# Performance work log

Hardware: AMD Instinct MI355X
Metric: run time of the kernel (lower is better)

## Reference

```python
import jax, jax.numpy as jnp
import numpy as np
import math

B, T, C, H, D, R = 1, 2048, 2048, 16, 128, 64
W_LOCAL = 512
DELTA_I = 0.75
ROPE_BASE = 10000.0


def _rotate(x):
    # interleaved rotate-half, exactly as in the torch source
    x1, x2 = x[..., ::2], x[..., 1::2]
    return jnp.stack((-x2, x1), axis=-1).reshape(x.shape)


def _rope_tables(seq_len):
    inv_freq = 1.0 / (ROPE_BASE ** (jnp.arange(0, D, 2, dtype=jnp.float32) / D))
    t = jnp.arange(seq_len, dtype=jnp.float32)
    freqs = jnp.einsum('i,j->ij', t, inv_freq)          # [T, D/2]
    emb = jnp.concatenate((freqs, freqs), axis=-1)      # [T, D] (half-layout, as in source)
    return jnp.cos(emb)[None, None], jnp.sin(emb)[None, None]


def setup_inputs() -> dict:
    key = jax.random.key(0)
    ks = jax.random.split(key, 8)
    s = 0.02
    return {
        'x': jax.random.normal(ks[0], (B, T, C), dtype=jnp.float32),
        'w_qkv': jax.random.normal(ks[1], (3 * C, C), dtype=jnp.float32) * s,
        'w_o': jax.random.normal(ks[2], (C, C), dtype=jnp.float32) * s,
        'pk': jax.random.normal(ks[3], (R, D), dtype=jnp.float32) * s,
        'pv': jax.random.normal(ks[4], (R, D), dtype=jnp.float32) * s,
        'uo': jax.random.normal(ks[5], (D, R), dtype=jnp.float32) * s,
        'info_w1': jax.random.normal(ks[6], (C // 4, C), dtype=jnp.float32) * s,
        'info_w2': jax.random.normal(ks[7], (1, C // 4), dtype=jnp.float32) * s,
    }


def reference(x, w_qkv, w_o, pk, pv, uo, info_w1, info_w2):
    Bx, Tx, Cx = x.shape
    scale = 1.0 / math.sqrt(D)

    qkv = x @ w_qkv.T                                   # [B,T,3C]
    q, k, v = jnp.split(qkv, 3, axis=-1)
    q = q.reshape(Bx, Tx, H, D).transpose(0, 2, 1, 3)   # [B,H,T,D]
    k = k.reshape(Bx, Tx, H, D).transpose(0, 2, 1, 3)
    v = v.reshape(Bx, Tx, H, D).transpose(0, 2, 1, 3)

    cos, sin = _rope_tables(Tx)
    q = q * cos + _rotate(q) * sin
    k = k * cos + _rotate(k) * sin

    # causal local-window attention (full [B,H,T,T] scores, as in source)
    w = min(W_LOCAL, Tx)
    idx = jnp.arange(Tx)
    rel = idx[None, :] - idx[:, None]                   # j - i
    local_mask = (rel > 0) | (rel < -(w - 1))           # True = masked
    scores = jnp.einsum('bhtd,bhsd->bhts', q, k) * scale
    scores = jnp.where(local_mask[None, None], -jnp.inf, scores)
    attn_local = jax.nn.softmax(scores, axis=-1)
    ctx_local = jnp.einsum('bhts,bhsd->bhtd', attn_local, v)

    # informational gate (no-grad path in source)
    h_info = jax.nn.gelu(x @ info_w1.T, approximate=False)
    info_score = jax.nn.sigmoid((h_info @ info_w2.T)[..., 0])   # [B,T]
    gate = (info_score > DELTA_I).astype(x.dtype)

    # low-rank global path (unmasked softmax over all tokens, as in source)
    k_r = jnp.einsum('bhsd,rd->bhsr', k, pk)
    v_r = jnp.einsum('bhsd,rd->bhsr', v, pv)
    q_r = jnp.einsum('bhtd,rd->bhtr', q, pk)
    scores_g = jnp.einsum('bhtr,bhsr->bhts', q_r, k_r) * (scale * D / R)
    attn_g = jax.nn.softmax(scores_g, axis=-1)
    ctx_g_r = jnp.einsum('bhts,bhsr->bhtr', attn_g, v_r)
    ctx_g = jnp.einsum('bhtr,dr->bhtd', ctx_g_r, uo)
    gate_q = gate[:, None, :, None]                     # [B,1,T,1]
    ctx = ctx_local + ctx_g * gate_q

    ctx = ctx.transpose(0, 2, 1, 3).reshape(Bx, Tx, Cx)
    return ctx @ w_o.T
```

## Files before the change

### kernel.cpp

```cpp
#include <hip/hip_runtime.h>
#include <hip/hip_bf16.h>
#include <math.h>

#define T_LEN 2048
#define C_DIM 2048
#define NH 16
#define HD 128
#define RANK 64
#define W_LOCAL 512
#define QKV_LD 6144
#define ROW_BF 12288
#define KB_OFF 4096
#define VB_OFF 8192
#define WO_OFF 6144
#define SCALE 0.08838834764831845f
#define SCALE_G 0.17677669529663687f
#define LOG1E4_OVER_64 0.14391156831212787f

typedef __bf16 bf16_t;
typedef __bf16 bf16x8 __attribute__((ext_vector_type(8)));
typedef __bf16 bf16x4 __attribute__((ext_vector_type(4)));
typedef float f32x4 __attribute__((ext_vector_type(4)));

__device__ __forceinline__ void async_copy16(const bf16_t* g, bf16_t* l) {
    __builtin_amdgcn_global_load_lds(
        (const __attribute__((address_space(1))) unsigned int*)g,
        (__attribute__((address_space(3))) unsigned int*)l, 16, 0, 0);
}

__global__ __launch_bounds__(256)
void prep_kernel(const float* __restrict__ x, bf16_t* __restrict__ xb,
                 const float* __restrict__ w_qkv, bf16_t* __restrict__ wqb,
                 float* __restrict__ tab) {
    const int bid = blockIdx.x;
    const int tid = threadIdx.x;
    if (bid < 2048) {
        int idx = bid * 256 + tid;
        const float* p = x + (size_t)idx * 8;
        float4 v0 = *(const float4*)p;
        float4 v1 = *(const float4*)(p + 4);
        bf16x8 o;
        o[0] = (bf16_t)v0.x; o[1] = (bf16_t)v0.y; o[2] = (bf16_t)v0.z; o[3] = (bf16_t)v0.w;
        o[4] = (bf16_t)v1.x; o[5] = (bf16_t)v1.y; o[6] = (bf16_t)v1.z; o[7] = (bf16_t)v1.w;
        *(bf16x8*)(xb + (size_t)idx * 8) = o;
    } else if (bid < 8192) {
        int idx = (bid - 2048) * 256 + tid;
        const float* p = w_qkv + (size_t)idx * 8;
        float4 v0 = *(const float4*)p;
        float4 v1 = *(const float4*)(p + 4);
        bf16x8 o;
        o[0] = (bf16_t)v0.x; o[1] = (bf16_t)v0.y; o[2] = (bf16_t)v0.z; o[3] = (bf16_t)v0.w;
        o[4] = (bf16_t)v1.x; o[5] = (bf16_t)v1.y; o[6] = (bf16_t)v1.z; o[7] = (bf16_t)v1.w;
        *(bf16x8*)(wqb + (size_t)idx * 8) = o;
    } else {
        int idx = (bid - 8192) * 256 + tid;
        int t = idx >> 6, j = idx & 63;
        float inv = expf(-(float)j * LOG1E4_OVER_64);
        float s, c;
        sincosf((float)t * inv, &s, &c);
        tab[t * 128 + j] = c;
        tab[t * 128 + 64 + j] = s;
    }
}

#define NTK 32
#define ILD 40

#define STG_A(bb, ktile) do {                                                  \
    _Pragma("unroll")                                                          \
    for (int c_ = 0; c_ < 4; ++c_)                                             \
        async_copy16(gA + (size_t)(c_ * 32) * 2048 + (ktile) * 64,             \
                     &lds[bb][0][(c_ * 32 + rS) * 64 + dS]);                   \
} while (0)

#define STG_B(bb, ktile) do {                                                  \
    _Pragma("unroll")                                                          \
    for (int c_ = 0; c_ < 4; ++c_)                                             \
        async_copy16(gB + (size_t)(c_ * 32) * 2048 + (ktile) * 64,             \
                     &lds[bb][1][(c_ * 32 + rS) * 64 + dS]);                   \
} while (0)

#define RD_A(bb, m, k) (*(const bf16x8*)&lds[bb][0][(wr * 64 + (m) * 16 + l16) * 64 + (((k) * 4 + quad) ^ xsw) * 8])
#define RD_B(bb, n, k) (*(const bf16x8*)&lds[bb][1][(wc * 64 + (n) * 16 + l16) * 64 + (((k) * 4 + quad) ^ xsw) * 8])

__global__ __launch_bounds__(256, 2)
void gemm_qkv_rope(const bf16_t* __restrict__ A, const bf16_t* __restrict__ B,
                   bf16_t* __restrict__ qkv_bf, bf16_t* __restrict__ vt,
                   const float* __restrict__ tab, const float* __restrict__ w_o,
                   const float* __restrict__ x, const float* __restrict__ w1,
                   float* __restrict__ ipart) {
    __shared__ __align__(16) unsigned char smem[65536];
    const int bid = blockIdx.x;
    const int tid = threadIdx.x;

    if (bid < 128) {
        bf16_t* Ah = (bf16_t*)smem;
        bf16_t* Al = Ah + 128 * ILD;
        bf16_t* Bh = Al + 128 * ILD;
        bf16_t* Bl = Bh + 128 * ILD;
        const int bn = bid & 3, bm = (bid >> 2) & 15, ks = bid >> 6;
        const int wave = tid >> 6, lane = tid & 63;
        const int quad = lane >> 4, l16 = lane & 15;
        const int wm = (wave >> 1) * 64, wn = (wave & 1) * 64;
        const int lrow = lane >> 2;
        const int lkb = (lane & 3) * 8;
        const int kbeg = ks * 1024;

        f32x4 acc[4][4];
#pragma unroll
        for (int i = 0; i < 4; ++i)
#pragma unroll
            for (int j = 0; j < 4; ++j) acc[i][j] = (f32x4){0.f, 0.f, 0.f, 0.f};

        const float* gx = x + (size_t)(bm * 128 + wave * 16 + lrow) * 2048 + kbeg + lkb;
        const float* gw = w1 + (size_t)(bn * 128 + wave * 16 + lrow) * 2048 + kbeg + lkb;
        const int wrow = (wave * 16 + lrow) * ILD + lkb;

        for (int k0 = 0; k0 < 1024; k0 += 32) {
            __syncthreads();
#pragma unroll
            for (int hr = 0; hr < 2; ++hr) {
                const float* px = gx + (size_t)hr * 64 * 2048 + k0;
                float4 a0 = *(const float4*)px, a1 = *(const float4*)(px + 4);
                float av[8] = {a0.x, a0.y, a0.z, a0.w, a1.x, a1.y, a1.z, a1.w};
                bf16x8 h, l;
#pragma unroll
                for (int i = 0; i < 8; ++i) {
                    bf16_t hb = (bf16_t)av[i];
                    h[i] = hb; l[i] = (bf16_t)(av[i] - (float)hb);
                }
                *(bf16x8*)&Ah[wrow + hr * 64 * ILD] = h;
                *(bf16x8*)&Al[wrow + hr * 64 * ILD] = l;

                const float* pw = gw + (size_t)hr * 64 * 2048 + k0;
                float4 b0 = *(const float4*)pw, b1 = *(const float4*)(pw + 4);
                float bv[8] = {b0.x, b0.y, b0.z, b0.w, b1.x, b1.y, b1.z, b1.w};
                bf16x8 hb2, lb2;
#pragma unroll
                for (int i = 0; i < 8; ++i) {
                    bf16_t hh = (bf16_t)bv[i];
                    hb2[i] = hh; lb2[i] = (bf16_t)(bv[i] - (float)hh);
                }
                *(bf16x8*)&Bh[wrow + hr * 64 * ILD] = hb2;
                *(bf16x8*)&Bl[wrow + hr * 64 * ILD] = lb2;
            }
            __syncthreads();

            bf16x8 ah[4], al[4], bh[4], bl[4];
#pragma unroll
            for (int mt = 0; mt < 4; ++mt) {
                ah[mt] = *(const bf16x8*)&Ah[(wm + mt * 16 + l16) * ILD + quad * 8];
                al[mt] = *(const bf16x8*)&Al[(wm + mt * 16 + l16) * ILD + quad * 8];
            }
#pragma unroll
            for (int nt = 0; nt < 4; ++nt) {
                bh[nt] = *(const bf16x8*)&Bh[(wn + nt * 16 + l16) * ILD + quad * 8];
                bl[nt] = *(const bf16x8*)&Bl[(wn + nt * 16 + l16) * ILD + quad * 8];
            }
#pragma unroll
            for (int mt = 0; mt < 4; ++mt)
#pragma unroll
                for (int nt = 0; nt < 4; ++nt) {
                    acc[mt][nt] = __builtin_amdgcn_mfma_f32_16x16x32_bf16(ah[mt], bh[nt], acc[mt][nt], 0, 0, 0);
                    acc[mt][nt] = __builtin_amdgcn_mfma_f32_16x16x32_bf16(ah[mt], bl[nt], acc[mt][nt], 0, 0, 0);
                    acc[mt][nt] = __builtin_amdgcn_mfma_f32_16x16x32_bf16(al[mt], bh[nt], acc[mt][nt], 0, 0, 0);
                }
        }

        float* cp = ipart + (size_t)ks * 2048 * 512;
#pragma unroll
        for (int mt = 0; mt < 4; ++mt)
#pragma unroll
            for (int r = 0; r < 4; ++r) {
                int row = bm * 128 + wm + mt * 16 + quad * 4 + r;
                float* crow = cp + (size_t)row * 512 + bn * 128 + wn;
#pragma unroll
                for (int nt = 0; nt < 4; ++nt)
                    crow[nt * 16 + l16] = acc[mt][nt][r];
            }
        return;
    }

    if (bid >= 896) {
        int row = bid - 896;
        int c = tid * 8;
        const float* p = w_o + (size_t)row * 2048 + c;
        float4 v0 = *(const float4*)p;
        float4 v1 = *(const float4*)(p + 4);
        bf16x8 o;
        o[0] = (bf16_t)v0.x; o[1] = (bf16_t)v0.y; o[2] = (bf16_t)v0.z; o[3] = (bf16_t)v0.w;
        o[4] = (bf16_t)v1.x; o[5] = (bf16_t)v1.y; o[6] = (bf16_t)v1.z; o[7] = (bf16_t)v1.w;
        *(bf16x8*)(qkv_bf + (size_t)row * ROW_BF + WO_OFF + c) = o;
        return;
    }

    typedef bf16_t ldsbuf_t[2][128 * 64];
    ldsbuf_t* lds = (ldsbuf_t*)smem;

    const int gid = bid - 128;
    const int xcd = gid & 7, idx = gid >> 3;
    const int bn_ = xcd * 6 + (idx % 6);
    const int bm_ = idx / 6;
    const int wave = tid >> 6, lane = tid & 63;
    const int quad = lane >> 4, l16 = lane & 15;
    const int wr = wave >> 1, wc = wave & 1;
    const int xsw = l16 & 7;

    const int rS = tid >> 3;
    const int cS = ((tid & 7) ^ (rS & 7)) * 8;
    const int dS = (tid & 7) * 8;
    const bf16_t* gA = A + (size_t)(bm_ * 128 + rS) * 2048 + cS;
    const bf16_t* gB = B + (size_t)(bn_ * 128 + rS) * 2048 + cS;

    f32x4 acc[4][4];
#pragma unroll
    for (int i = 0; i < 4; ++i)
#pragma unroll
        for (int j = 0; j < 4; ++j) acc[i][j] = (f32x4){0.f, 0.f, 0.f, 0.f};

    STG_A(0, 0); STG_B(0, 0);
    STG_A(1, 1); STG_B(1, 1);
    asm volatile("s_waitcnt vmcnt(8)" ::: "memory");
    __builtin_amdgcn_s_barrier();

    for (int kt = 0; kt < NTK; ++kt) {
        const int b = kt & 1;
        bf16x8 af[4][2], bfr[4][2];
#pragma unroll
        for (int m = 0; m < 4; ++m) { af[m][0] = RD_A(b, m, 0); af[m][1] = RD_A(b, m, 1); }
#pragma unroll
        for (int n = 0; n < 4; ++n) { bfr[n][0] = RD_B(b, n, 0); bfr[n][1] = RD_B(b, n, 1); }
        asm volatile("s_waitcnt lgkmcnt(0)" ::: "memory");
        __builtin_amdgcn_s_barrier();

        __builtin_amdgcn_s_setprio(1);
#pragma unroll
        for (int m = 0; m < 4; ++m)
#pragma unroll
            for (int n = 0; n < 4; ++n)
                acc[m][n] = __builtin_amdgcn_mfma_f32_16x16x32_bf16(af[m][0], bfr[n][0], acc[m][n], 0, 0, 0);
        __builtin_amdgcn_s_setprio(0);
        if (kt + 2 < NTK) STG_A(b, kt + 2);

        __builtin_amdgcn_s_setprio(1);
#pragma unroll
        for (int m = 0; m < 4; ++m)
#pragma unroll
            for (int n = 0; n < 4; ++n)
                acc[m][n] = __builtin_amdgcn_mfma_f32_16x16x32_bf16(af[m][1], bfr[n][1], acc[m][n], 0, 0, 0);
        __builtin_amdgcn_s_setprio(0);
        if (kt + 2 < NTK) STG_B(b, kt + 2);

        if (kt < NTK - 2) { asm volatile("s_waitcnt vmcnt(8)" ::: "memory"); }
        else              { asm volatile("s_waitcnt vmcnt(0)" ::: "memory"); }
        __builtin_amdgcn_s_barrier();
    }

    const int colbase = bn_ * 128 + wc * 64;
    const int region = (bn_ * 128) >> 11;
    const int rowbase = bm_ * 128 + wr * 64;
    const bool odd = (l16 & 1);

    if (region == 2) {
#pragma unroll
        for (int mt = 0; mt < 4; ++mt)
#pragma unroll
            for (int r = 0; r < 4; ++r) {
                int t = rowbase + mt * 16 + quad * 4 + r;
                bf16_t* brow = qkv_bf + (size_t)t * ROW_BF + VB_OFF + (colbase - 4096);
#pragma unroll
                for (int nt = 0; nt < 4; ++nt)
                    brow[nt * 16 + l16] = (bf16_t)acc[mt][nt][r];
            }
        bf16_t* Tl = (bf16_t*)smem;
#pragma unroll
        for (int mt = 0; mt < 4; ++mt)
#pragma unroll
            for (int r = 0; r < 4; ++r) {
                int rloc = wr * 64 + mt * 16 + quad * 4 + r;
#pragma unroll
                for (int nt = 0; nt < 4; ++nt) {
                    int cloc = wc * 64 + nt * 16 + l16;
                    Tl[cloc * 136 + rloc] = (bf16_t)acc[mt][nt][r];
                }
            }
        __syncthreads();
        const int hh = bn_ - 32;
        const int d = tid >> 1, th = (tid & 1) * 64;
        bf16_t* dst = vt + ((size_t)(hh * 128 + d)) * 2048 + bm_ * 128 + th;
        const bf16_t* srcT = Tl + d * 136 + th;
#pragma unroll
        for (int j = 0; j < 8; ++j)
            *(bf16x8*)(dst + j * 8) = *(const bf16x8*)(srcT + j * 8);
    } else {
#pragma unroll
        for (int mt = 0; mt < 4; ++mt)
#pragma unroll
            for (int r = 0; r < 4; ++r) {
                int t = rowbase + mt * 16 + quad * 4 + r;
                const float* trow = tab + t * 128;
#pragma unroll
                for (int nt = 0; nt < 4; ++nt) {
                    float v = acc[mt][nt][r];
                    float vp = __shfl_xor(v, 1);
                    int col = colbase + nt * 16 + l16;
                    int j = col & 63;
                    float c = trow[j], s = trow[64 + j];
                    float y = odd ? (v * c + vp * s) : (v * c - vp * s);
                    qkv_bf[(size_t)t * ROW_BF + (region == 0 ? col : col + 2048)] = (bf16_t)y;
                }
            }
    }
}

#define STG_A3(bb, ktile) do {                                                 \
    _Pragma("unroll")                                                          \
    for (int c_ = 0; c_ < 4; ++c_)                                             \
        async_copy16(gA + (size_t)(c_ * 32) * 2048 + (ktile) * 64,             \
                     &ldsA[bb][(c_ * 32 + rS) * 64 + dS]);                     \
} while (0)

#define STG_B3(bb, ktile) do {                                                 \
    _Pragma("unroll")                                                          \
    for (int c_ = 0; c_ < 2; ++c_)                                             \
        async_copy16(gB + (size_t)(c_ * 32) * ROW_BF + (ktile) * 64,           \
                     &ldsB[bb][(c_ * 32 + rS) * 64 + dS]);                     \
} while (0)

#define RD_A3(bb, m, k) (*(const bf16x8*)&ldsA[bb][(wr * 64 + (m) * 16 + l16) * 64 + (((k) * 4 + quad) ^ xsw) * 8])
#define RD_B3(bb, n, k) (*(const bf16x8*)&ldsB[bb][(wc * 32 + (n) * 16 + l16) * 64 + (((k) * 4 + quad) ^ xsw) * 8])

__global__ __launch_bounds__(256, 2)
void gemm_ctx_wo(const bf16_t* __restrict__ A, const bf16_t* __restrict__ Bov,
                 float* __restrict__ C) {
    __shared__ __align__(16) bf16_t ldsA[2][128 * 64];
    __shared__ __align__(16) bf16_t ldsB[2][64 * 64];

    const int bid = blockIdx.x;
    const int xcd = bid & 7, idx = bid >> 3;
    const int bn_ = xcd * 4 + (idx & 3);
    const int bm_ = idx >> 2;
    const int tid = threadIdx.x;
    const int wave = tid >> 6, lane = tid & 63;
    const int quad = lane >> 4, l16 = lane & 15;
    const int wr = wave >> 1, wc = wave & 1;
    const int xsw = l16 & 7;

    const int rS = tid >> 3;
    const int cS = ((tid & 7) ^ (rS & 7)) * 8;
    const int dS = (tid & 7) * 8;
    const bf16_t* gA = A + (size_t)(bm_ * 128 + rS) * 2048 + cS;
    const bf16_t* gB = Bov + (size_t)(bn_ * 64 + rS) * ROW_BF + cS;

    f32x4 acc[4][2];
#pragma unroll
    for (int i = 0; i < 4; ++i)
#pragma unroll
        for (int j = 0; j < 2; ++j) acc[i][j] = (f32x4){0.f, 0.f, 0.f, 0.f};

    STG_A3(0, 0); STG_B3(0, 0);
    STG_A3(1, 1); STG_B3(1, 1);
    asm volatile("s_waitcnt vmcnt(6)" ::: "memory");
    __builtin_amdgcn_s_barrier();

    for (int kt = 0; kt < NTK; ++kt) {
        const int b = kt & 1;
        bf16x8 af[4][2], bfr[2][2];
#pragma unroll
        for (int m = 0; m < 4; ++m) { af[m][0] = RD_A3(b, m, 0); af[m][1] = RD_A3(b, m, 1); }
#pragma unroll
        for (int n = 0; n < 2; ++n) { bfr[n][0] = RD_B3(b, n, 0); bfr[n][1] = RD_B3(b, n, 1); }
        asm volatile("s_waitcnt lgkmcnt(0)" ::: "memory");
        __builtin_amdgcn_s_barrier();

        __builtin_amdgcn_s_setprio(1);
#pragma unroll
        for (int m = 0; m < 4; ++m)
#pragma unroll
            for (int n = 0; n < 2; ++n)
                acc[m][n] = __builtin_amdgcn_mfma_f32_16x16x32_bf16(af[m][0], bfr[n][0], acc[m][n], 0, 0, 0);
        __builtin_amdgcn_s_setprio(0);
        if (kt + 2 < NTK) STG_A3(b, kt + 2);

        __builtin_amdgcn_s_setprio(1);
#pragma unroll
        for (int m = 0; m < 4; ++m)
#pragma unroll
            for (int n = 0; n < 2; ++n)
                acc[m][n] = __builtin_amdgcn_mfma_f32_16x16x32_bf16(af[m][1], bfr[n][1], acc[m][n], 0, 0, 0);
        __builtin_amdgcn_s_setprio(0);
        if (kt + 2 < NTK) STG_B3(b, kt + 2);

        if (kt < NTK - 2) { asm volatile("s_waitcnt vmcnt(6)" ::: "memory"); }
        else              { asm volatile("s_waitcnt vmcnt(0)" ::: "memory"); }
        __builtin_amdgcn_s_barrier();
    }

    const int colbase = bn_ * 64 + wc * 32;
    const int rowbase = bm_ * 128 + wr * 64;
#pragma unroll
    for (int mt = 0; mt < 4; ++mt)
#pragma unroll
        for (int r = 0; r < 4; ++r) {
            int row = rowbase + mt * 16 + quad * 4 + r;
            float* crow = C + (size_t)row * 2048 + colbase;
#pragma unroll
            for (int nt = 0; nt < 2; ++nt)
                crow[nt * 16 + l16] = acc[mt][nt][r];
        }
}

__device__ __forceinline__ float gelu_exact(float v) {
    return 0.5f * v * (1.0f + erff(v * 0.70710678118654752f));
}

#define QTI 64
#define KTI 64
#define PS_LD 72
#define KV_LD 136

__global__ __launch_bounds__(256, 2)
void attn_fused(const bf16_t* __restrict__ qkv_bf, const bf16_t* __restrict__ vt,
                bf16_t* __restrict__ cxb,
                const float* __restrict__ pk, const float* __restrict__ pv,
                float* __restrict__ kr, float* __restrict__ vr,
                bf16_t* __restrict__ qr,
                const float* __restrict__ Cpart, const float* __restrict__ w2,
                float* __restrict__ gate) {
    __shared__ __align__(16) unsigned char smem[58368];
    const int bid = blockIdx.x;
    const int tid = threadIdx.x;
    const int wave = tid >> 6, lane = tid & 63;
    const int quad = lane >> 4, l16 = lane & 15;

    if (bid >= 1024) {
        const int t = (bid - 1024) * 4 + wave;
        const float* p0 = Cpart + (size_t)t * 512;
        float s = 0.f;
#pragma unroll
        for (int i = lane; i < 512; i += 64) {
            float v = p0[i] + p0[i + 1048576];
            s += gelu_exact(v) * w2[i];
        }
#pragma unroll
        for (int off = 32; off > 0; off >>= 1) s += __shfl_down(s, off);
        if (lane == 0) {
            float sig = 1.f / (1.f + expf(-s));
            gate[t] = (sig > 0.75f) ? 1.f : 0.f;
        }
        return;
    }

    if (bid >= 512) {
        bf16_t* Pk = (bf16_t*)smem;
        bf16_t* Pv = Pk + 64 * KV_LD;
        bf16_t* Op = Pv + 64 * KV_LD;
        const int i0 = bid - 512;
        const int h = i0 >> 5, s0 = (i0 & 31) * 64;

#pragma unroll
        for (int i = 0; i < 8; ++i) {
            int gid = i * 256 + tid;
            int row = gid >> 5, c = (gid & 31) << 2;
            float4 wk = *(const float4*)(pk + (size_t)row * HD + c);
            float4 wv = *(const float4*)(pv + (size_t)row * HD + c);
            bf16x4 qk4, qv4;
            qk4[0] = (bf16_t)wk.x; qk4[1] = (bf16_t)wk.y; qk4[2] = (bf16_t)wk.z; qk4[3] = (bf16_t)wk.w;
            qv4[0] = (bf16_t)wv.x; qv4[1] = (bf16_t)wv.y; qv4[2] = (bf16_t)wv.z; qv4[3] = (bf16_t)wv.w;
            *(bf16x4*)&Pk[row * KV_LD + c] = qk4;
            *(bf16x4*)&Pv[row * KV_LD + c] = qv4;
        }

        f32x4 ak[4], av[4], aq[4];
#pragma unroll
        for (int nt = 0; nt < 4; ++nt) {
            ak[nt] = (f32x4){0.f, 0.f, 0.f, 0.f};
            av[nt] = (f32x4){0.f, 0.f, 0.f, 0.f};
            aq[nt] = (f32x4){0.f, 0.f, 0.f, 0.f};
        }

#pragma unroll
        for (int i = 0; i < 4; ++i) {
            int gid = i * 256 + tid;
            int row = gid >> 4, ch = (gid & 15) << 3;
            *(bf16x8*)&Op[row * KV_LD + ch] =
                *(const bf16x8*)(qkv_bf + (size_t)(s0 + row) * ROW_BF + KB_OFF + h * HD + ch);
        }
        __syncthreads();
#pragma unroll
        for (int ks = 0; ks < 4; ++ks) {
            bf16x8 a = *(const bf16x8*)&Op[(wave * 16 + l16) * KV_LD + ks * 32 + quad * 8];
#pragma unroll
            for (int nt = 0; nt < 4; ++nt) {
                bf16x8 bk = *(const bf16x8*)&Pk[(nt * 16 + l16) * KV_LD + ks * 32 + quad * 8];
                ak[nt] = __builtin_amdgcn_mfma_f32_16x16x32_bf16(a, bk, ak[nt], 0, 0, 0);
            }
        }
        __syncthreads();
#pragma unroll
        for (int i = 0; i < 4; ++i) {
            int gid = i * 256 + tid;
            int row = gid >> 4, ch = (gid & 15) << 3;
            *(bf16x8*)&Op[row * KV_LD + ch] =
                *(const bf16x8*)(qkv_bf + (size_t)(s0 + row) * ROW_BF + VB_OFF + h * HD + ch);
        }
        __syncthreads();
#pragma unroll
        for (int ks = 0; ks < 4; ++ks) {
            bf16x8 a = *(const bf16x8*)&Op[(wave * 16 + l16) * KV_LD + ks * 32 + quad * 8];
#pragma unroll
            for (int nt = 0; nt < 4; ++nt) {
                bf16x8 bv = *(const bf16x8*)&Pv[(nt * 16 + l16) * KV_LD + ks * 32 + quad * 8];
                av[nt] = __builtin_amdgcn_mfma_f32_16x16x32_bf16(a, bv, av[nt], 0, 0, 0);
            }
        }
        __syncthreads();
#pragma unroll
        for (int i = 0; i < 4; ++i) {
            int gid = i * 256 + tid;
            int row = gid >> 4, ch = (gid & 15) << 3;
            *(bf16x8*)&Op[row * KV_LD + ch] =
                *(const bf16x8*)(qkv_bf + (size_t)(s0 + row) * ROW_BF + h * HD + ch);
        }
        __syncthreads();
#pragma unroll
        for (int ks = 0; ks < 4; ++ks) {
            bf16x8 a = *(const bf16x8*)&Op[(wave * 16 + l16) * KV_LD + ks * 32 + quad * 8];
#pragma unroll
            for (int nt = 0; nt < 4; ++nt) {
                bf16x8 bk = *(const bf16x8*)&Pk[(nt * 16 + l16) * KV_LD + ks * 32 + quad * 8];
                aq[nt] = __builtin_amdgcn_mfma_f32_16x16x32_bf16(a, bk, aq[nt], 0, 0, 0);
            }
        }

#pragma unroll
        for (int nt = 0; nt < 4; ++nt)
#pragma unroll
            for (int r = 0; r < 4; ++r) {
                int s = s0 + wave * 16 + quad * 4 + r;
                size_t idx = ((size_t)h * T_LEN + s) * RANK + nt * 16 + l16;
                kr[idx] = ak[nt][r];
                vr[idx] = av[nt][r];
                qr[idx] = (bf16_t)aq[nt][r];
            }
        return;
    }

    bf16_t* Qs  = (bf16_t*)smem;
    bf16_t* Ks  = Qs + QTI * 128;
    bf16_t* Vts = Ks + KTI * 128;
    bf16_t* Psb = Vts + 128 * KTI;

    const int h = bid >> 5;
    const int t0 = (bid & 31) * QTI;
    const int xsw = l16 & 7;

    const bf16_t* vth = vt + (size_t)h * 128 * 2048;

#pragma unroll
    for (int i = 0; i < 4; ++i) {
        int c = i * 256 + tid;
        int row = c >> 4, pc = c & 15;
        int lc = pc ^ (row & 7);
        async_copy16(qkv_bf + (size_t)(t0 + row) * ROW_BF + h * HD + lc * 8, &Qs[c * 8]);
    }

    f32x4 o[8];
#pragma unroll
    for (int d8 = 0; d8 < 8; ++d8) o[d8] = (f32x4){0.f, 0.f, 0.f, 0.f};
    float m_i[4] = {-1e30f, -1e30f, -1e30f, -1e30f};
    float l_i[4] = {0.f, 0.f, 0.f, 0.f};

    __syncthreads();

    for (int kt = 0; kt < 9; ++kt) {
        const int sbase = t0 - 512 + kt * KTI;
        if (sbase < 0) continue;
        __syncthreads();
#pragma unroll
        for (int i = 0; i < 4; ++i) {
            int c = i * 256 + tid;
            int row = c >> 4, pc = c & 15;
            int lc = pc ^ (row & 7);
            async_copy16(qkv_bf + (size_t)(sbase + row) * ROW_BF + KB_OFF + h * HD + lc * 8,
                         &Ks[c * 8]);
        }
#pragma unroll
        for (int i = 0; i < 4; ++i) {
            int c = i * 256 + tid;
            int row = c >> 3, pc = c & 7;
            int lc = pc ^ (row & 7);
            async_copy16(vth + (size_t)row * 2048 + sbase + lc * 8, &Vts[c * 8]);
        }
        __syncthreads();

        f32x4 sacc[4];
#pragma unroll
        for (int nt = 0; nt < 4; ++nt) sacc[nt] = (f32x4){0.f, 0.f, 0.f, 0.f};
#pragma unroll
        for (int ks = 0; ks < 4; ++ks) {
            bf16x8 a = *(const bf16x8*)&Qs[(wave * 16 + l16) * 128 + (((ks * 4 + quad) ^ xsw)) * 8];
#pragma unroll
            for (int nt = 0; nt < 4; ++nt) {
                bf16x8 b = *(const bf16x8*)&Ks[(nt * 16 + l16) * 128 + (((ks * 4 + quad) ^ xsw)) * 8];
                sacc[nt] = __builtin_amdgcn_mfma_f32_16x16x32_bf16(a, b, sacc[nt], 0, 0, 0);
            }
        }

#pragma unroll
        for (int nt = 0; nt < 4; ++nt)
#pragma unroll
            for (int r = 0; r < 4; ++r) sacc[nt][r] *= SCALE;

        if (kt == 0 || kt == 8) {
#pragma unroll
            for (int nt = 0; nt < 4; ++nt) {
                int s_g = sbase + nt * 16 + l16;
#pragma unroll
                for (int r = 0; r < 4; ++r) {
                    int t_g = t0 + wave * 16 + quad * 4 + r;
                    bool valid = (s_g <= t_g) && (s_g + W_LOCAL > t_g);
                    if (!valid) sacc[nt][r] = -1e30f;
                }
            }
        }

#pragma unroll
        for (int r = 0; r < 4; ++r) {
            float mx = fmaxf(fmaxf(sacc[0][r], sacc[1][r]), fmaxf(sacc[2][r], sacc[3][r]));
            mx = fmaxf(mx, __shfl_xor(mx, 1));
            mx = fmaxf(mx, __shfl_xor(mx, 2));
            mx = fmaxf(mx, __shfl_xor(mx, 4));
            mx = fmaxf(mx, __shfl_xor(mx, 8));
            float mnew = fmaxf(m_i[r], mx);
            float alpha = __expf(m_i[r] - mnew);
            m_i[r] = mnew;
            float rs = 0.f;
#pragma unroll
            for (int nt = 0; nt < 4; ++nt) {
                float p = __expf(sacc[nt][r] - mnew);
                sacc[nt][r] = p;
                rs += p;
            }
            rs += __shfl_xor(rs, 1);
            rs += __shfl_xor(rs, 2);
            rs += __shfl_xor(rs, 4);
            rs += __shfl_xor(rs, 8);
            l_i[r] = l_i[r] * alpha + rs;
#pragma unroll
            for (int d8 = 0; d8 < 8; ++d8) o[d8][r] *= alpha;
        }

#pragma unroll
        for (int r = 0; r < 4; ++r)
#pragma unroll
            for (int nt = 0; nt < 4; ++nt)
                Psb[wave * 16 * PS_LD + (quad * 4 + r) * PS_LD + nt * 16 + l16] = (bf16_t)sacc[nt][r];

#pragma unroll
        for (int ks2 = 0; ks2 < 2; ++ks2) {
            bf16x8 a = *(const bf16x8*)&Psb[wave * 16 * PS_LD + l16 * PS_LD + ks2 * 32 + quad * 8];
#pragma unroll
            for (int d8 = 0; d8 < 8; ++d8) {
                int rw = d8 * 16 + l16;
                bf16x8 b = *(const bf16x8*)&Vts[rw * 64 + (((ks2 * 4 + quad) ^ xsw)) * 8];
                o[d8] = __builtin_amdgcn_mfma_f32_16x16x32_bf16(a, b, o[d8], 0, 0, 0);
            }
        }
    }

#pragma unroll
    for (int r = 0; r < 4; ++r) {
        float inv = 1.0f / l_i[r];
        size_t rowoff = (size_t)(t0 + wave * 16 + quad * 4 + r) * 2048 + h * HD;
#pragma unroll
        for (int d8 = 0; d8 < 8; ++d8)
            cxb[rowoff + d8 * 16 + l16] = (bf16_t)(o[d8][r] * inv);
    }
}

__device__ __forceinline__ float block_reduce_max512(float v, float* red, int tid) {
    red[tid] = v; __syncthreads();
    for (int s = 256; s > 0; s >>= 1) {
        if (tid < s) red[tid] = fmaxf(red[tid], red[tid + s]);
        __syncthreads();
    }
    float r = red[0]; __syncthreads();
    return r;
}
__device__ __forceinline__ float block_reduce_sum512(float v, float* red, int tid) {
    red[tid] = v; __syncthreads();
    for (int s = 256; s > 0; s >>= 1) {
        if (tid < s) red[tid] = red[tid] + red[tid + s];
        __syncthreads();
    }
    float r = red[0]; __syncthreads();
    return r;
}

__global__ __launch_bounds__(512)
void global_attn_kernel(bf16_t* __restrict__ cxb, const float* __restrict__ kr,
                        const float* __restrict__ vr, const bf16_t* __restrict__ qr,
                        const float* __restrict__ uo, const float* __restrict__ gate) {
    const int t = blockIdx.x, h = blockIdx.y;
    if (gate[t] <= 0.5f) return;

    __shared__ float qrs[64];
    __shared__ float red[512];
    __shared__ float cgr[64];
    __shared__ float sg[2048];
    const int tid = threadIdx.x;

    if (tid < 64) qrs[tid] = (float)qr[((size_t)h * T_LEN + t) * RANK + tid];
    __syncthreads();

    const float* krh = kr + (size_t)h * T_LEN * RANK;
    const float* vrh = vr + (size_t)h * T_LEN * RANK;
    float lmax = -INFINITY;
    for (int s = tid; s < T_LEN; s += 512) {
        const float* krr = krh + (size_t)s * RANK;
        float acc = 0.f;
#pragma unroll
        for (int r = 0; r < RANK; r += 4) {
            float4 k4 = *(const float4*)(krr + r);
            acc += qrs[r] * k4.x + qrs[r + 1] * k4.y + qrs[r + 2] * k4.z + qrs[r + 3] * k4.w;
        }
        float sc = acc * SCALE_G;
        sg[s] = sc;
        lmax = fmaxf(lmax, sc);
    }
    float gmx = block_reduce_max512(lmax, red, tid);
    float lsum = 0.f;
    for (int s = tid; s < T_LEN; s += 512) {
        float pp = expf(sg[s] - gmx);
        sg[s] = pp;
        lsum += pp;
    }
    float gsum = block_reduce_sum512(lsum, red, tid);

    {
        const int r = tid & 63, part = tid >> 6;
        float pacc = 0.f;
        for (int s = part; s < T_LEN; s += 8) pacc += sg[s] * vrh[(size_t)s * RANK + r];
        red[tid] = pacc;
        __syncthreads();
        if (tid < 64) {
            float c = 0.f;
#pragma unroll
            for (int pp = 0; pp < 8; ++pp) c += red[pp * 64 + tid];
            cgr[tid] = c / gsum;
        }
        __syncthreads();
    }

    if (tid < 128) {
        float cg = 0.f;
#pragma unroll
        for (int r = 0; r < RANK; ++r) cg += cgr[r] * uo[tid * RANK + r];
        size_t off = (size_t)t * 2048 + h * HD + tid;
        cxb[off] = (bf16_t)((float)cxb[off] + cg);
    }
}

extern "C" void kernel_launch(void* const* d_in, const int* in_sizes, int n_in,
                              void* d_out, int out_size, void* d_ws, size_t ws_size,
                              hipStream_t stream) {
    const float* x     = (const float*)d_in[0];
    const float* w_qkv = (const float*)d_in[1];
    const float* w_o   = (const float*)d_in[2];
    const float* pk    = (const float*)d_in[3];
    const float* pv    = (const float*)d_in[4];
    const float* uo    = (const float*)d_in[5];
    const float* w1    = (const float*)d_in[6];
    const float* w2    = (const float*)d_in[7];
    float* out = (float*)d_out;

    float* ws = (float*)d_ws;
    float* qkv   = ws;
    float* hinfo = qkv + (size_t)12582912;
    float* gatep = hinfo + (size_t)1048576;
    bf16_t* xb   = (bf16_t*)(gatep + 2048);
    float* wqbf  = gatep + 2048 + 2097152;
    bf16_t* wqb  = (bf16_t*)wqbf;
    float* krp   = wqbf;
    float* vrp   = wqbf + (size_t)2097152;
    float* tabp  = hinfo;
    bf16_t* qrp  = (bf16_t*)hinfo;
    bf16_t* cxb  = xb;
    bf16_t* qkvb = (bf16_t*)qkv;
    bf16_t* wob  = qkvb + WO_OFF;
    bf16_t* vtp  = (bf16_t*)d_out;
    float* ipart = (float*)(vtp + (size_t)16 * 128 * 2048);

    prep_kernel<<<8704, 256, 0, stream>>>(x, xb, w_qkv, wqb, tabp);
    gemm_qkv_rope<<<2944, 256, 0, stream>>>(xb, wqb, qkvb, vtp, tabp, w_o, x, w1, ipart);
    attn_fused<<<1536, 256, 0, stream>>>(qkvb, vtp, cxb, pk, pv, krp, vrp, qrp,
                                         ipart, w2, gatep);
    global_attn_kernel<<<dim3(T_LEN, NH), 512, 0, stream>>>(cxb, krp, vrp, qrp, uo, gatep);
    gemm_ctx_wo<<<512, 256, 0, stream>>>(cxb, wob, out);
}
```

Measured before the change: 281.0 us.

## Double-buffer K/V tiles in local attention and keep Q in registers

The local-window attention loop now double-buffers the K and V^T shared-memory tiles, so the async copy of tile j+2 is issued while tile j+1's data is already resident. Waits use vmcnt-based partial counts plus raw barriers. Q fragments are loaded straight from global memory into registers instead of being staged through LDS, which frees LDS for the second buffer. The start tile is computed up front so invalid early tiles are skipped without a per-iteration test. Risks: shared memory grows to about 73 KB, which may limit blocks per CU, and the extra Q registers add pressure under launch_bounds(256,2).

```diff
diff --git a/kernel.cpp b/kernel.cpp
--- a/kernel.cpp
+++ b/kernel.cpp
@@ -419,6 +419,25 @@
 #define PS_LD 72
 #define KV_LD 136
 
+#define STG_KV(Kdst, Vdst, sb_) do {                                           \
+    _Pragma("unroll")                                                          \
+    for (int i_ = 0; i_ < 4; ++i_) {                                           \
+        int c_ = i_ * 256 + tid;                                               \
+        int row_ = c_ >> 4, pc_ = c_ & 15;                                     \
+        int lc_ = pc_ ^ (row_ & 7);                                            \
+        async_copy16(qkv_bf + (size_t)((sb_) + row_) * ROW_BF + KB_OFF + h * HD + lc_ * 8, \
+                     (Kdst) + c_ * 8);                                         \
+    }                                                                          \
+    _Pragma("unroll")                                                          \
+    for (int i_ = 0; i_ < 4; ++i_) {                                           \
+        int c_ = i_ * 256 + tid;                                               \
+        int row_ = c_ >> 3, pc_ = c_ & 7;                                      \
+        int lc_ = pc_ ^ (row_ & 7);                                            \
+        async_copy16(vth + (size_t)row_ * 2048 + (sb_) + lc_ * 8,              \
+                     (Vdst) + c_ * 8);                                         \
+    }                                                                          \
+} while (0)
+
 __global__ __launch_bounds__(256, 2)
 void attn_fused(const bf16_t* __restrict__ qkv_bf, const bf16_t* __restrict__ vt,
                 bf16_t* __restrict__ cxb,
@@ -427,7 +446,7 @@
                 bf16_t* __restrict__ qr,
                 const float* __restrict__ Cpart, const float* __restrict__ w2,
                 float* __restrict__ gate) {
-    __shared__ __align__(16) unsigned char smem[58368];
+    __shared__ __align__(16) unsigned char smem[74752];
     const int bid = blockIdx.x;
     const int tid = threadIdx.x;
     const int wave = tid >> 6, lane = tid & 63;
@@ -546,24 +565,27 @@
         return;
     }
 
-    bf16_t* Qs  = (bf16_t*)smem;
-    bf16_t* Ks  = Qs + QTI * 128;
-    bf16_t* Vts = Ks + KTI * 128;
-    bf16_t* Psb = Vts + 128 * KTI;
+    bf16_t* Ks  = (bf16_t*)smem;
+    bf16_t* Vts = Ks + 2 * (KTI * 128);
+    bf16_t* Psb = Vts + 2 * (128 * KTI);
 
     const int h = bid >> 5;
     const int t0 = (bid & 31) * QTI;
     const int xsw = l16 & 7;
-
     const bf16_t* vth = vt + (size_t)h * 128 * 2048;
 
-#pragma unroll
-    for (int i = 0; i < 4; ++i) {
-        int c = i * 256 + tid;
-        int row = c >> 4, pc = c & 15;
-        int lc = pc ^ (row & 7);
-        async_copy16(qkv_bf + (size_t)(t0 + row) * ROW_BF + h * HD + lc * 8, &Qs[c * 8]);
-    }
+    const int ktst = (t0 >= 512) ? 0 : (8 - (t0 >> 6));
+    const int nval = 9 - ktst;
+    const int sb0 = t0 - 512 + ktst * KTI;
+
+    bf16x8 qreg[4];
+    {
+        const bf16_t* qrow = qkv_bf + (size_t)(t0 + wave * 16 + l16) * ROW_BF + h * HD + quad * 8;
+#pragma unroll
+        for (int ks = 0; ks < 4; ++ks)
+            qreg[ks] = *(const bf16x8*)(qrow + ks * 32);
+    }
+    asm volatile("s_waitcnt vmcnt(0)" ::: "memory");
 
     f32x4 o[8];
 #pragma unroll
@@ -571,39 +593,30 @@
     float m_i[4] = {-1e30f, -1e30f, -1e30f, -1e30f};
     float l_i[4] = {0.f, 0.f, 0.f, 0.f};
 
-    __syncthreads();
-
-    for (int kt = 0; kt < 9; ++kt) {
-        const int sbase = t0 - 512 + kt * KTI;
-        if (sbase < 0) continue;
-        __syncthreads();
-#pragma unroll
-        for (int i = 0; i < 4; ++i) {
-            int c = i * 256 + tid;
-            int row = c >> 4, pc = c & 15;
-            int lc = pc ^ (row & 7);
-            async_copy16(qkv_bf + (size_t)(sbase + row) * ROW_BF + KB_OFF + h * HD + lc * 8,
-                         &Ks[c * 8]);
-        }
-#pragma unroll
-        for (int i = 0; i < 4; ++i) {
-            int c = i * 256 + tid;
-            int row = c >> 3, pc = c & 7;
-            int lc = pc ^ (row & 7);
-            async_copy16(vth + (size_t)row * 2048 + sbase + lc * 8, &Vts[c * 8]);
-        }
-        __syncthreads();
+    STG_KV(Ks, Vts, sb0);
+    if (nval > 1) {
+        STG_KV(Ks + KTI * 128, Vts + 128 * KTI, sb0 + KTI);
+        asm volatile("s_waitcnt vmcnt(8)" ::: "memory");
+    } else {
+        asm volatile("s_waitcnt vmcnt(0)" ::: "memory");
+    }
+    __builtin_amdgcn_s_barrier();
+
+    for (int j = 0; j < nval; ++j) {
+        const int b = j & 1;
+        const int sbase = sb0 + j * KTI;
+        bf16_t* KsB = Ks + b * (KTI * 128);
+        bf16_t* VtB = Vts + b * (128 * KTI);
 
         f32x4 sacc[4];
 #pragma unroll
         for (int nt = 0; nt < 4; ++nt) sacc[nt] = (f32x4){0.f, 0.f, 0.f, 0.f};
 #pragma unroll
         for (int ks = 0; ks < 4; ++ks) {
-            bf16x8 a = *(const bf16x8*)&Qs[(wave * 16 + l16) * 128 + (((ks * 4 + quad) ^ xsw)) * 8];
 #pragma unroll
             for (int nt = 0; nt < 4; ++nt) {
-                bf16x8 b = *(const bf16x8*)&Ks[(nt * 16 + l16) * 128 + (((ks * 4 + quad) ^ xsw)) * 8];
-                sacc[nt] = __builtin_amdgcn_mfma_f32_16x16x32_bf16(a, b, sacc[nt], 0, 0, 0);
+                bf16x8 bb = *(const bf16x8*)&KsB[(nt * 16 + l16) * 128 + (((ks * 4 + quad) ^ xsw)) * 8];
+                sacc[nt] = __builtin_amdgcn_mfma_f32_16x16x32_bf16(qreg[ks], bb, sacc[nt], 0, 0, 0);
             }
         }
 
@@ -612,7 +625,7 @@
 #pragma unroll
             for (int r = 0; r < 4; ++r) sacc[nt][r] *= SCALE;
 
-        if (kt == 0 || kt == 8) {
+        if ((j == 0 && ktst == 0) || (j == nval - 1)) {
 #pragma unroll
             for (int nt = 0; nt < 4; ++nt) {
                 int s_g = sbase + nt * 16 + l16;
@@ -663,10 +676,20 @@
 #pragma unroll
             for (int d8 = 0; d8 < 8; ++d8) {
                 int rw = d8 * 16 + l16;
-                bf16x8 b = *(const bf16x8*)&Vts[rw * 64 + (((ks2 * 4 + quad) ^ xsw)) * 8];
-                o[d8] = __builtin_amdgcn_mfma_f32_16x16x32_bf16(a, b, o[d8], 0, 0, 0);
-            }
-        }
+                bf16x8 bb = *(const bf16x8*)&VtB[rw * 64 + (((ks2 * 4 + quad) ^ xsw)) * 8];
+                o[d8] = __builtin_amdgcn_mfma_f32_16x16x32_bf16(a, bb, o[d8], 0, 0, 0);
+            }
+        }
+
+        asm volatile("s_waitcnt lgkmcnt(0)" ::: "memory");
+        __builtin_amdgcn_s_barrier();
+        if (j + 2 < nval) {
+            STG_KV(KsB, VtB, sbase + 2 * KTI);
+            asm volatile("s_waitcnt vmcnt(8)" ::: "memory");
+        } else {
+            asm volatile("s_waitcnt vmcnt(0)" ::: "memory");
+        }
+        __builtin_amdgcn_s_barrier();
     }
 
 #pragma unroll
```

Measured after the change: 283.5 us. About the same (+0.9%).
